# Performance work log

Measured on AMD Instinct MI355X. Metric: run time of the kernel, lower is better.

## Reference

```python
import jax, jax.numpy as jnp
import numpy as np

B, POMO, PROB, EMB, H, D = 64, 200, 200, 512, 16, 32
SQRT_EMB = 22.627416997969522  # sqrt(512)
CLIP = 10.0


def _heads(x):
    # (b, n, H*D) -> (b, H, n, D)
    b, n, _ = x.shape
    return x.reshape(b, n, H, D).transpose(0, 2, 1, 3)


def setup_inputs() -> dict:
    key = jax.random.key(0)
    ks = jax.random.split(key, 10)
    s = 1.0 / np.sqrt(EMB)
    return {
        "encoded_nodes": jax.random.normal(ks[0], (B, PROB + 1, EMB), jnp.float32),
        "encoded_q1": jax.random.normal(ks[1], (B, POMO, EMB), jnp.float32),
        "encoded_last_node": jax.random.normal(ks[2], (B, POMO, EMB), jnp.float32),
        "ninf_mask": jnp.zeros((B, POMO, PROB), jnp.float32),
        "Wq_first": jax.random.normal(ks[3], (EMB, H * D), jnp.float32) * s,
        "Wq_last": jax.random.normal(ks[4], (EMB, H * D), jnp.float32) * s,
        "Wk": jax.random.normal(ks[5], (EMB, H * D), jnp.float32) * s,
        "Wv": jax.random.normal(ks[6], (EMB, H * D), jnp.float32) * s,
        "Wc": jax.random.normal(ks[7], (H * D, EMB), jnp.float32) * s,
        "bc": jax.random.normal(ks[8], (EMB,), jnp.float32) * 0.01,
    }


def reference(encoded_nodes, encoded_q1, encoded_last_node, ninf_mask,
              Wq_first, Wq_last, Wk, Wv, Wc, bc):
    # set_kv
    k = _heads(encoded_nodes @ Wk)            # (b, H, prob+1, D)
    v = _heads(encoded_nodes @ Wv)            # (b, H, prob+1, D)
    single_head_key = encoded_nodes[:, :-1]   # (b, prob, emb)
    # set_q1 + forward queries
    q = _heads(encoded_q1 @ Wq_first) + _heads(encoded_last_node @ Wq_last)  # (b, H, pomo, D)
    # masked multi-head attention; mask padded with a zero column for the depot/last node
    mask3 = jnp.concatenate([ninf_mask, jnp.zeros((B, POMO, 1), ninf_mask.dtype)], axis=-1)
    score = jnp.einsum('bhnd,bhmd->bhnm', q, k) / jnp.sqrt(jnp.float32(D))
    weights = jax.nn.softmax(score + mask3[:, None, :, :], axis=-1)
    out = jnp.einsum('bhnm,bhmd->bhnd', weights, v)        # (b, H, pomo, D)
    out_concat = out.transpose(0, 2, 1, 3).reshape(B, POMO, H * D)
    mh_atten_out = out_concat @ Wc + bc                    # (b, pomo, emb)
    # single-head pointer score with tanh clipping
    score2 = jnp.einsum('bne,bpe->bnp', mh_atten_out, single_head_key) / SQRT_EMB
    score_masked = CLIP * jnp.tanh(score2) + ninf_mask
    return jax.nn.softmax(score_masked, axis=2)            # (b, pomo, prob)
```

## Files before the change

kernel.cpp:

```cpp
#include <hip/hip_runtime.h>
#include <cstdint>
#include <cstddef>

typedef _Float16 f16;
typedef f16 f16x4 __attribute__((ext_vector_type(4)));
typedef f16 f16x8 __attribute__((ext_vector_type(8)));
typedef float f32x4 __attribute__((ext_vector_type(4)));

#define NB    64
#define NPOMO 200
#define NNODE 201
#define NEMB  512
#define NH    16
#define ND    32

__device__ __forceinline__ void gload16(const void* g, void* l) {
  __builtin_amdgcn_global_load_lds((const __attribute__((address_space(1))) void*)g,
                                   (__attribute__((address_space(3))) void*)l, 16, 0, 0);
}


__global__ void cast_x(const float* __restrict__ x, f16* __restrict__ o, int n4) {
  int i = blockIdx.x * 256 + threadIdx.x;
  if (i < n4) {
    float4 v = ((const float4*)x)[i];
    f16x4 h = {(f16)v.x, (f16)v.y, (f16)v.z, (f16)v.w};
    ((f16x4*)o)[i] = h;
  }
}

__global__ void build_qcat(const float* __restrict__ q1, const float* __restrict__ ql,
                           f16* __restrict__ o) {
  int i = blockIdx.x * 256 + threadIdx.x;
  if (i >= 12800 * 256) return;
  int row = i >> 8;
  int g = i & 255;
  const float* src = (g < 128) ? (q1 + (size_t)row * 512 + g * 4)
                               : (ql + (size_t)row * 512 + (g - 128) * 4);
  float4 v = *(const float4*)src;
  f16x4 h = {(f16)v.x, (f16)v.y, (f16)v.z, (f16)v.w};
  ((f16x4*)o)[i] = h;
}

__global__ void build_w(const float* __restrict__ Wk, const float* __restrict__ Wv,
                        const float* __restrict__ Wqf, const float* __restrict__ Wql,
                        const float* __restrict__ Wc,
                        f16* __restrict__ wkvT, f16* __restrict__ wqT, f16* __restrict__ wcT) {
  int i = blockIdx.x * 256 + threadIdx.x;
  if (i < 524288) {
    int j = i >> 9, k = i & 511;
    float v = (j < 512) ? Wk[(size_t)k * 512 + j] : Wv[(size_t)k * 512 + (j - 512)];
    wkvT[i] = (f16)v;
  } else if (i < 1048576) {
    int t = i - 524288;
    int j = t >> 10, k = t & 1023;
    float v = (k < 512) ? Wqf[(size_t)k * 512 + j] : Wql[(size_t)(k - 512) * 512 + j];
    wqT[t] = (f16)v;
  } else if (i < 1310720) {
    int t = i - 1048576;
    int j = t >> 9, k = t & 511;
    wcT[t] = (f16)Wc[(size_t)k * 512 + j];
  }
}


__global__ __launch_bounds__(256, 2) void gemm_tn(
    const f16* __restrict__ A, const f16* __restrict__ B, f16* __restrict__ C,
    const float* __restrict__ bias, int M, int N, int K) {
  __shared__ f16 As[128 * 64];
  __shared__ f16 Bs[128 * 64];
  const int tid = threadIdx.x;
  const int wave = tid >> 6, lane = tid & 63;
  const int qd = lane >> 4, c = lane & 15;
  const int wm = wave >> 1, wn = wave & 1;
  const int m0 = blockIdx.x * 128, n0 = blockIdx.y * 128;
  const int srow = lane >> 3, sj = lane & 7;

  f32x4 acc[4][4];
#pragma unroll
  for (int i = 0; i < 4; ++i)
#pragma unroll
    for (int j = 0; j < 4; ++j) acc[i][j] = (f32x4){0.f, 0.f, 0.f, 0.f};

  for (int kc = 0; kc < K; kc += 64) {
#pragma unroll
    for (int i = 0; i < 4; ++i) {
      int row = wave * 32 + i * 8 + srow;
      int gr = m0 + row; if (gr >= M) gr = M - 1;
      int gj = sj ^ (row & 7);
      gload16(A + (size_t)gr * K + kc + gj * 8, As + row * 64 + sj * 8);
    }
#pragma unroll
    for (int i = 0; i < 4; ++i) {
      int row = wave * 32 + i * 8 + srow;
      int gj = sj ^ (row & 7);
      gload16(B + (size_t)(n0 + row) * K + kc + gj * 8, Bs + row * 64 + sj * 8);
    }
    __syncthreads();
#pragma unroll
    for (int kk = 0; kk < 2; ++kk) {
      f16x8 af[4], bf[4];
#pragma unroll
      for (int t = 0; t < 4; ++t) {
        int ra = wm * 64 + t * 16 + c;
        af[t] = *(const f16x8*)(As + ra * 64 + (((kk * 4 + qd) ^ (ra & 7)) * 8));
        int rb = wn * 64 + t * 16 + c;
        bf[t] = *(const f16x8*)(Bs + rb * 64 + (((kk * 4 + qd) ^ (rb & 7)) * 8));
      }
#pragma unroll
      for (int mt = 0; mt < 4; ++mt)
#pragma unroll
        for (int nt = 0; nt < 4; ++nt)
          acc[mt][nt] = __builtin_amdgcn_mfma_f32_16x16x32_f16(af[mt], bf[nt], acc[mt][nt], 0, 0, 0);
    }
    __syncthreads();
  }

#pragma unroll
  for (int mt = 0; mt < 4; ++mt) {
#pragma unroll
    for (int nt = 0; nt < 4; ++nt) {
      int col = n0 + wn * 64 + nt * 16 + c;
      float bv = bias ? bias[col] : 0.0f;
#pragma unroll
      for (int r = 0; r < 4; ++r) {
        int row = m0 + wm * 64 + mt * 16 + qd * 4 + r;
        if (row < M) C[(size_t)row * N + col] = (f16)(acc[mt][nt][r] + bv);
      }
    }
  }
}


#define VSTR 268

__global__ __launch_bounds__(256, 4) void attn_kernel(
    const f16* __restrict__ Qp, const f16* __restrict__ KV,
    const float* __restrict__ mask, f16* __restrict__ Oc) {
  __shared__ f16 Vt[32 * VSTR];
  const int bid = blockIdx.x;
  const int qq = bid & 3;
  const int h = (bid >> 2) & 15;
  const int b = bid >> 6;
  const int tid = threadIdx.x;
  const int wave = tid >> 6, lane = tid & 63;
  const int qd = lane >> 4, c = lane & 15;

  for (int idx = tid; idx < 208 * 8; idx += 256) {
    int m = idx >> 3, ch = idx & 7;
    f16x4 v = (f16x4){0, 0, 0, 0};
    if (m < 201) v = *(const f16x4*)(KV + ((size_t)(b * NNODE + m)) * 1024 + 512 + h * 32 + ch * 4);
    Vt[(ch * 4 + 0) * VSTR + m] = v.x;
    Vt[(ch * 4 + 1) * VSTR + m] = v.y;
    Vt[(ch * 4 + 2) * VSTR + m] = v.z;
    Vt[(ch * 4 + 3) * VSTR + m] = v.w;
  }
  __syncthreads();

  const int start = (qq == 0) ? 0 : (1 + 3 * qq);
  const int ntile = (qq == 0) ? 4 : 3;
  const int rt = start + wave;
  if (wave >= ntile) return;

  const int r0 = rt * 16;
  const int qrow = min(r0 + c, 199);
  const float scale = 0.17677669529663687f;

  f16x8 aq = *(const f16x8*)(Qp + ((size_t)(b * NPOMO + qrow)) * 512 + h * 32 + qd * 8);

  f32x4 s[13];
#pragma unroll
  for (int nt = 0; nt < 13; ++nt) {
    int node = nt * 16 + c; if (node > 200) node = 200;
    f16x8 ak = *(const f16x8*)(KV + ((size_t)(b * NNODE + node)) * 1024 + h * 32 + qd * 8);
    f32x4 z = (f32x4){0.f, 0.f, 0.f, 0.f};
    s[nt] = __builtin_amdgcn_mfma_f32_16x16x32_f16(ak, aq, z, 0, 0, 0);
  }

  float mx = -3e38f;
#pragma unroll
  for (int nt = 0; nt < 13; ++nt) {
    const int col0 = nt * 16 + qd * 4;
    float4 mv = make_float4(0.f, 0.f, 0.f, 0.f);
    if (col0 < 200)
      mv = *(const float4*)(mask + ((size_t)b * NPOMO + qrow) * 200 + col0);
#pragma unroll
    for (int r = 0; r < 4; ++r) {
      int node = col0 + r;
      float v;
      if (node > 200)      v = -3e38f;
      else if (node == 200) v = s[nt][r] * scale;
      else                  v = s[nt][r] * scale + ((const float*)&mv)[r];
      s[nt][r] = v;
      mx = fmaxf(mx, v);
    }
  }
  mx = fmaxf(mx, __shfl_xor(mx, 16));
  mx = fmaxf(mx, __shfl_xor(mx, 32));

  float sm = 0.f;
  f16x4 pf[13];
#pragma unroll
  for (int nt = 0; nt < 13; ++nt) {
    f16x4 p4;
#pragma unroll
    for (int r = 0; r < 4; ++r) {
      float p = __expf(s[nt][r] - mx);
      sm += p;
      p4[r] = (f16)p;
    }
    pf[nt] = p4;
  }
  sm += __shfl_xor(sm, 16);
  sm += __shfl_xor(sm, 32);
  const float inv = 1.0f / sm;

  f32x4 o0 = (f32x4){0.f, 0.f, 0.f, 0.f};
  f32x4 o1 = (f32x4){0.f, 0.f, 0.f, 0.f};
#pragma unroll
  for (int nt = 0; nt < 13; ++nt) {
    const int nb = nt * 16 + qd * 4;
    f16x4 av0 = *(const f16x4*)(Vt + c * VSTR + nb);
    f16x4 av1 = *(const f16x4*)(Vt + (c + 16) * VSTR + nb);
    o0 = __builtin_amdgcn_mfma_f32_16x16x16f16(av0, pf[nt], o0, 0, 0, 0);
    o1 = __builtin_amdgcn_mfma_f32_16x16x16f16(av1, pf[nt], o1, 0, 0, 0);
  }

  const int row = r0 + c;
  if (row < 200) {
    f16* dst = Oc + ((size_t)(b * NPOMO + row)) * 512 + h * 32 + qd * 4;
    f16x4 w0 = {(f16)(o0[0] * inv), (f16)(o0[1] * inv), (f16)(o0[2] * inv), (f16)(o0[3] * inv)};
    f16x4 w1 = {(f16)(o1[0] * inv), (f16)(o1[1] * inv), (f16)(o1[2] * inv), (f16)(o1[3] * inv)};
    *(f16x4*)dst = w0;
    *(f16x4*)(dst + 16) = w1;
  }
}


__global__ __launch_bounds__(256, 4) void final_kernel(
    const f16* __restrict__ mh, const f16* __restrict__ Xnh,
    const float* __restrict__ mask, float* __restrict__ out) {
  __shared__ float xmax[4][16];
  __shared__ float xsum[4][16];
  const int b = blockIdx.x / 13;
  const int tile = blockIdx.x % 13;
  const int r0 = tile * 16;
  const int tid = threadIdx.x;
  const int wave = tid >> 6, lane = tid & 63;
  const int qd = lane >> 4, c = lane & 15;

  const int nt0 = (wave == 0) ? 0 : (3 * wave + 1);
  const int cnt = (wave == 0) ? 4 : 3;

  const int qrow = min(r0 + c, 199);
  const size_t rbase = ((size_t)(b * NPOMO + qrow)) * 512;

  size_t abase[4];
#pragma unroll
  for (int i = 0; i < 4; ++i) {
    int nt = nt0 + i;
    int nd = nt * 16 + c; if (nd > 200) nd = 200;
    abase[i] = ((size_t)(b * NNODE + nd)) * 512;
  }

  f32x4 acc[4];
#pragma unroll
  for (int i = 0; i < 4; ++i) acc[i] = (f32x4){0.f, 0.f, 0.f, 0.f};

#pragma unroll 4
  for (int kc = 0; kc < 512; kc += 32) {
    f16x8 bq = *(const f16x8*)(mh + rbase + kc + qd * 8);
#pragma unroll
    for (int i = 0; i < 4; ++i) {
      if (i < cnt) {
        f16x8 a = *(const f16x8*)(Xnh + abase[i] + kc + qd * 8);
        acc[i] = __builtin_amdgcn_mfma_f32_16x16x32_f16(a, bq, acc[i], 0, 0, 0);
      }
    }
  }

  const float invS = 1.0f / 22.627416997969522f;
  float mx = -3e38f;
#pragma unroll
  for (int i = 0; i < 4; ++i) {
    if (i >= cnt) break;
    const int nt = nt0 + i;
    const int col0 = nt * 16 + qd * 4;
    float4 mv = make_float4(0.f, 0.f, 0.f, 0.f);
    if (col0 < 200)
      mv = *(const float4*)(mask + ((size_t)b * NPOMO + qrow) * 200 + col0);
#pragma unroll
    for (int r = 0; r < 4; ++r) {
      int node = col0 + r;
      float v;
      if (node < 200) {
        float t = __expf(2.0f * acc[i][r] * invS);
        float th = 1.0f - 2.0f / (t + 1.0f);
        v = 10.0f * th + ((const float*)&mv)[r];
      } else {
        v = -3e38f;
      }
      acc[i][r] = v;
      mx = fmaxf(mx, v);
    }
  }
  mx = fmaxf(mx, __shfl_xor(mx, 16));
  mx = fmaxf(mx, __shfl_xor(mx, 32));
  if (lane < 16) xmax[wave][lane] = mx;
  __syncthreads();
  mx = fmaxf(fmaxf(xmax[0][c], xmax[1][c]), fmaxf(xmax[2][c], xmax[3][c]));

  float sm = 0.f;
#pragma unroll
  for (int i = 0; i < 4; ++i) {
    if (i >= cnt) break;
#pragma unroll
    for (int r = 0; r < 4; ++r) {
      float p = __expf(acc[i][r] - mx);
      acc[i][r] = p;
      sm += p;
    }
  }
  sm += __shfl_xor(sm, 16);
  sm += __shfl_xor(sm, 32);
  if (lane < 16) xsum[wave][lane] = sm;
  __syncthreads();
  const float tot = xsum[0][c] + xsum[1][c] + xsum[2][c] + xsum[3][c];
  const float inv = 1.0f / tot;

  const int row = r0 + c;
  if (row < 200) {
#pragma unroll
    for (int i = 0; i < 4; ++i) {
      if (i >= cnt) break;
      const int col0 = (nt0 + i) * 16 + qd * 4;
      if (col0 < 200) {
        float4 o;
        o.x = acc[i][0] * inv; o.y = acc[i][1] * inv;
        o.z = acc[i][2] * inv; o.w = acc[i][3] * inv;
        *(float4*)(out + ((size_t)b * NPOMO + row) * 200 + col0) = o;
      }
    }
  }
}


extern "C" void kernel_launch(void* const* d_in, const int* in_sizes, int n_in,
                              void* d_out, int out_size, void* d_ws, size_t ws_size,
                              hipStream_t stream) {
  (void)in_sizes; (void)n_in; (void)out_size; (void)ws_size;
  const float* enc   = (const float*)d_in[0];
  const float* q1    = (const float*)d_in[1];
  const float* qlast = (const float*)d_in[2];
  const float* mask  = (const float*)d_in[3];
  const float* Wqf   = (const float*)d_in[4];
  const float* Wql   = (const float*)d_in[5];
  const float* Wk    = (const float*)d_in[6];
  const float* Wv    = (const float*)d_in[7];
  const float* Wc    = (const float*)d_in[8];
  const float* bc    = (const float*)d_in[9];
  float* out = (float*)d_out;

  char* ws = (char*)d_ws;
  f16* Xnh  = (f16*)(ws + 0);
  f16* Qcat = (f16*)(ws + 13172736);
  f16* WkvT = (f16*)(ws + 39387136);
  f16* WqT  = (f16*)(ws + 40435712);
  f16* WcT  = (f16*)(ws + 41484288);
  f16* KVp  = (f16*)(ws + 42008576);
  f16* Qp   = (f16*)(ws + 68354048);
  f16* Oc   = (f16*)(ws + 81461248);
  f16* mhb  = (f16*)(ws + 94568448);

  hipLaunchKernelGGL(cast_x, dim3(6432), dim3(256), 0, stream, enc, Xnh, 1646592);
  hipLaunchKernelGGL(build_qcat, dim3(12800), dim3(256), 0, stream, q1, qlast, Qcat);
  hipLaunchKernelGGL(build_w, dim3(5120), dim3(256), 0, stream, Wk, Wv, Wqf, Wql, Wc, WkvT, WqT, WcT);
  hipLaunchKernelGGL(gemm_tn, dim3(101, 8), dim3(256), 0, stream,
                     Xnh, WkvT, KVp, (const float*)nullptr, 12864, 1024, 512);
  hipLaunchKernelGGL(gemm_tn, dim3(100, 4), dim3(256), 0, stream,
                     Qcat, WqT, Qp, (const float*)nullptr, 12800, 512, 1024);
  hipLaunchKernelGGL(attn_kernel, dim3(4096), dim3(256), 0, stream, Qp, KVp, mask, Oc);
  hipLaunchKernelGGL(gemm_tn, dim3(100, 4), dim3(256), 0, stream,
                     Oc, WcT, mhb, bc, 12800, 512, 512);
  hipLaunchKernelGGL(final_kernel, dim3(832), dim3(256), 0, stream, mhb, Xnh, mask, out);
}
```

Baseline: 316.2 us.

## Merge prep kernels and projection GEMMs into single launches; reorder attention grid

The three cast/transpose kernels become one prep kernel dispatched by block range, and the KV and Q projection GEMMs are combined into one launch by splitting the block index space. The attention kernel's block index now puts the head in the high bits so neighbouring blocks share a head across batches, and its occupancy hint rises from 4 to 6 blocks. The goal is fewer launches and less tail idle time between small kernels, at the risk of register pressure from the tighter launch bounds and a changed cache access pattern.

```diff
diff --git a/kernel.cpp b/kernel.cpp
--- a/kernel.cpp
+++ b/kernel.cpp
@@ -20,60 +20,59 @@
 }
 
 
-__global__ void cast_x(const float* __restrict__ x, f16* __restrict__ o, int n4) {
-  int i = blockIdx.x * 256 + threadIdx.x;
-  if (i < n4) {
-    float4 v = ((const float4*)x)[i];
+__global__ void prep_kernel(const float* __restrict__ enc, const float* __restrict__ q1,
+                            const float* __restrict__ ql, const float* __restrict__ Wk,
+                            const float* __restrict__ Wv, const float* __restrict__ Wqf,
+                            const float* __restrict__ Wql, const float* __restrict__ Wc,
+                            f16* __restrict__ Xnh, f16* __restrict__ Qcat,
+                            f16* __restrict__ wkvT, f16* __restrict__ wqT,
+                            f16* __restrict__ wcT) {
+  const int bx = blockIdx.x;
+  const int tid = threadIdx.x;
+  if (bx < 6432) {
+    int i = bx * 256 + tid;
+    if (i < 1646592) {
+      float4 v = ((const float4*)enc)[i];
+      f16x4 h = {(f16)v.x, (f16)v.y, (f16)v.z, (f16)v.w};
+      ((f16x4*)Xnh)[i] = h;
+    }
+  } else if (bx < 19232) {
+    int i = (bx - 6432) * 256 + tid;
+    int row = i >> 8;
+    int g = i & 255;
+    const float* src = (g < 128) ? (q1 + (size_t)row * 512 + g * 4)
+                                 : (ql + (size_t)row * 512 + (g - 128) * 4);
+    float4 v = *(const float4*)src;
     f16x4 h = {(f16)v.x, (f16)v.y, (f16)v.z, (f16)v.w};
-    ((f16x4*)o)[i] = h;
-  }
-}
-
-__global__ void build_qcat(const float* __restrict__ q1, const float* __restrict__ ql,
-                           f16* __restrict__ o) {
-  int i = blockIdx.x * 256 + threadIdx.x;
-  if (i >= 12800 * 256) return;
-  int row = i >> 8;
-  int g = i & 255;
-  const float* src = (g < 128) ? (q1 + (size_t)row * 512 + g * 4)
-                               : (ql + (size_t)row * 512 + (g - 128) * 4);
-  float4 v = *(const float4*)src;
-  f16x4 h = {(f16)v.x, (f16)v.y, (f16)v.z, (f16)v.w};
-  ((f16x4*)o)[i] = h;
-}
-
-__global__ void build_w(const float* __restrict__ Wk, const float* __restrict__ Wv,
-                        const float* __restrict__ Wqf, const float* __restrict__ Wql,
-                        const float* __restrict__ Wc,
-                        f16* __restrict__ wkvT, f16* __restrict__ wqT, f16* __restrict__ wcT) {
-  int i = blockIdx.x * 256 + threadIdx.x;
-  if (i < 524288) {
-    int j = i >> 9, k = i & 511;
-    float v = (j < 512) ? Wk[(size_t)k * 512 + j] : Wv[(size_t)k * 512 + (j - 512)];
-    wkvT[i] = (f16)v;
-  } else if (i < 1048576) {
-    int t = i - 524288;
-    int j = t >> 10, k = t & 1023;
-    float v = (k < 512) ? Wqf[(size_t)k * 512 + j] : Wql[(size_t)(k - 512) * 512 + j];
-    wqT[t] = (f16)v;
-  } else if (i < 1310720) {
-    int t = i - 1048576;
-    int j = t >> 9, k = t & 511;
-    wcT[t] = (f16)Wc[(size_t)k * 512 + j];
-  }
-}
-
-
-__global__ __launch_bounds__(256, 2) void gemm_tn(
+    ((f16x4*)Qcat)[i] = h;
+  } else {
+    int i = (bx - 19232) * 256 + tid;
+    if (i < 524288) {
+      int j = i >> 9, k = i & 511;
+      float v = (j < 512) ? Wk[(size_t)k * 512 + j] : Wv[(size_t)k * 512 + (j - 512)];
+      wkvT[i] = (f16)v;
+    } else if (i < 1048576) {
+      int t = i - 524288;
+      int j = t >> 10, k = t & 1023;
+      float v = (k < 512) ? Wqf[(size_t)k * 512 + j] : Wql[(size_t)(k - 512) * 512 + j];
+      wqT[t] = (f16)v;
+    } else if (i < 1310720) {
+      int t = i - 1048576;
+      int j = t >> 9, k = t & 511;
+      wcT[t] = (f16)Wc[(size_t)k * 512 + j];
+    }
+  }
+}
+
+
+__device__ __forceinline__ void gemm_body(
     const f16* __restrict__ A, const f16* __restrict__ B, f16* __restrict__ C,
-    const float* __restrict__ bias, int M, int N, int K) {
-  __shared__ f16 As[128 * 64];
-  __shared__ f16 Bs[128 * 64];
+    const float* __restrict__ bias, int M, int N, int K, int m0, int n0,
+    f16* As, f16* Bs) {
   const int tid = threadIdx.x;
   const int wave = tid >> 6, lane = tid & 63;
   const int qd = lane >> 4, c = lane & 15;
   const int wm = wave >> 1, wn = wave & 1;
-  const int m0 = blockIdx.x * 128, n0 = blockIdx.y * 128;
   const int srow = lane >> 3, sj = lane & 7;
 
   f32x4 acc[4][4];
@@ -131,17 +130,41 @@
   }
 }
 
+__global__ __launch_bounds__(256, 2) void gemm_proj(
+    const f16* __restrict__ Xnh, const f16* __restrict__ WkvT, f16* __restrict__ KVp,
+    const f16* __restrict__ Qcat, const f16* __restrict__ WqT, f16* __restrict__ Qp) {
+  __shared__ f16 As[128 * 64];
+  __shared__ f16 Bs[128 * 64];
+  const int bx = blockIdx.x;
+  if (bx < 808) {
+    gemm_body(Xnh, WkvT, KVp, nullptr, 12864, 1024, 512, (bx % 101) * 128, (bx / 101) * 128, As, Bs);
+  } else {
+    int t = bx - 808;
+    gemm_body(Qcat, WqT, Qp, nullptr, 12800, 512, 1024, (t % 100) * 128, (t / 100) * 128, As, Bs);
+  }
+}
+
+__global__ __launch_bounds__(256, 2) void gemm_wc(
+    const f16* __restrict__ Oc, const f16* __restrict__ WcT, f16* __restrict__ mhb,
+    const float* __restrict__ bc) {
+  __shared__ f16 As[128 * 64];
+  __shared__ f16 Bs[128 * 64];
+  const int bx = blockIdx.x;
+  gemm_body(Oc, WcT, mhb, bc, 12800, 512, 512, (bx % 100) * 128, (bx / 100) * 128, As, Bs);
+}
+
 
 #define VSTR 268
 
-__global__ __launch_bounds__(256, 4) void attn_kernel(
+__global__ __launch_bounds__(256, 6) void attn_kernel(
     const f16* __restrict__ Qp, const f16* __restrict__ KV,
     const float* __restrict__ mask, f16* __restrict__ Oc) {
   __shared__ f16 Vt[32 * VSTR];
   const int bid = blockIdx.x;
-  const int qq = bid & 3;
-  const int h = (bid >> 2) & 15;
-  const int b = bid >> 6;
+  const int b4q = bid & 255;
+  const int h = bid >> 8;
+  const int b = b4q >> 2;
+  const int qq = b4q & 3;
   const int tid = threadIdx.x;
   const int wave = tid >> 6, lane = tid & 63;
   const int qd = lane >> 4, c = lane & 15;
@@ -372,15 +395,11 @@
   f16* Oc   = (f16*)(ws + 81461248);
   f16* mhb  = (f16*)(ws + 94568448);
 
-  hipLaunchKernelGGL(cast_x, dim3(6432), dim3(256), 0, stream, enc, Xnh, 1646592);
-  hipLaunchKernelGGL(build_qcat, dim3(12800), dim3(256), 0, stream, q1, qlast, Qcat);
-  hipLaunchKernelGGL(build_w, dim3(5120), dim3(256), 0, stream, Wk, Wv, Wqf, Wql, Wc, WkvT, WqT, WcT);
-  hipLaunchKernelGGL(gemm_tn, dim3(101, 8), dim3(256), 0, stream,
-                     Xnh, WkvT, KVp, (const float*)nullptr, 12864, 1024, 512);
-  hipLaunchKernelGGL(gemm_tn, dim3(100, 4), dim3(256), 0, stream,
-                     Qcat, WqT, Qp, (const float*)nullptr, 12800, 512, 1024);
+  hipLaunchKernelGGL(prep_kernel, dim3(24352), dim3(256), 0, stream,
+                     enc, q1, qlast, Wk, Wv, Wqf, Wql, Wc, Xnh, Qcat, WkvT, WqT, WcT);
+  hipLaunchKernelGGL(gemm_proj, dim3(1208), dim3(256), 0, stream,
+                     Xnh, WkvT, KVp, Qcat, WqT, Qp);
   hipLaunchKernelGGL(attn_kernel, dim3(4096), dim3(256), 0, stream, Qp, KVp, mask, Oc);
-  hipLaunchKernelGGL(gemm_tn, dim3(100, 4), dim3(256), 0, stream,
-                     Oc, WcT, mhb, bc, 12800, 512, 512);
+  hipLaunchKernelGGL(gemm_wc, dim3(400), dim3(256), 0, stream, Oc, WcT, mhb, bc);
   hipLaunchKernelGGL(final_kernel, dim3(832), dim3(256), 0, stream, mhb, Xnh, mask, out);
 }
```

Measured after the change: 322.1 us. Within noise of the previous version (+1.9%).
